# Kernel tuning notes

Hardware: AMD Instinct MI355X
Metric: run time of the kernel (lower is better)

## Reference

```python
import jax, jax.numpy as jnp
import numpy as np
import math

NB_STEPS = 50          # quadrature sub-intervals -> 51 Clenshaw-Curtis points
NUM_RNN_STEPS = 2


def _cc_weights(nb_steps):
    # Faithful port of UMNN's compute_cc_weights (Clenshaw-Curtis quadrature).
    lam = np.arange(0, nb_steps + 1).reshape(-1, 1).astype(np.float64)
    lam = np.cos((lam @ lam.T) * math.pi / nb_steps)
    lam[:, 0] = 0.5
    lam[:, -1] = 0.5 * lam[:, -1]
    lam = lam * 2.0 / nb_steps
    W = np.arange(0, nb_steps + 1).reshape(-1, 1).astype(np.float64)
    W[np.arange(1, nb_steps + 1, 2)] = 0
    W = 2.0 / (1.0 - W ** 2)
    W[0] = 1.0
    W[np.arange(1, nb_steps + 1, 2)] = 0
    cc = (lam.T @ W).astype(np.float32).reshape(-1)                      # [S]
    steps = np.cos(np.arange(0, nb_steps + 1) * math.pi / nb_steps).astype(np.float32)  # [S]
    return jnp.asarray(cc), jnp.asarray(steps)

CC_W, CC_STEPS = _cc_weights(NB_STEPS)  # S = NB_STEPS + 1 = 51


def _integrand(t, h, W1, b1, W2, b2, W3, b3, final_w):
    # IntegrandNN: MLP(cat(t,h)) -> ELU + 1 (>=0) -> fused power features -> ReLU(Linear)
    z = jnp.concatenate([t, h], axis=1)          # [N, in_d]
    z = jax.nn.relu(z @ W1.T + b1)               # [N, 128]
    z = jax.nn.relu(z @ W2.T + b2)               # [N, 128]
    z = jax.nn.elu(z @ W3.T + b3) + 1.0          # [N, 1], >= 0
    p = jnp.concatenate([z ** 1.5, z ** 2, z ** 2.5, z ** 3, z ** 3.5], axis=1)  # [N, 5]
    return jax.nn.relu((1.0 / (p + 1.0)) @ final_w.T)  # [N, 1]


def _inner_integral(x, h, params):
    # InnerUMNN: integral of IntegrandNN from x to xmax, xmax = max(x) + 10 (global scalar)
    N = x.shape[0]
    S = NB_STEPS + 1
    xmax = jnp.max(x) + 10.0
    T = x + (xmax - x) * (CC_STEPS[None, :] + 1.0) * 0.5   # [N, S]
    Tf = T.reshape(N * S, 1)
    hf = jnp.broadcast_to(h[:, None, :], (N, S, h.shape[1])).reshape(N * S, -1)
    g = _integrand(Tf, hf, *params).reshape(N, S)
    z = jnp.sum(g * CC_W[None, :], axis=1, keepdims=True)  # [N, 1]
    return z * (xmax - x) * 0.5


def _outer_integral(xT, h, params):
    # ParallelNeuralIntegral of InnerUMNN from x0 = 0 to xT; xT: [B, 1]
    B = xT.shape[0]
    S = NB_STEPS + 1
    X = xT * (CC_STEPS[None, :] + 1.0) * 0.5               # [B, S] (x0 = 0)
    Xf = X.reshape(B * S, 1)
    hf = jnp.broadcast_to(h[:, None, :], (B, S, h.shape[1])).reshape(B * S, -1)
    f = _inner_integral(Xf, hf, params).reshape(B, S)      # nested quadrature
    z = jnp.sum(f * CC_W[None, :], axis=1, keepdims=True)  # [B, 1]
    return z * xT * 0.5


def setup_inputs() -> dict:
    key = jax.random.key(0)
    ks = jax.random.split(key, 8)
    B, NF, IN_D, H = 256, 512, 64, 128
    x_ = jax.random.normal(ks[0], (B, NF), jnp.float32)
    h_ = jax.random.normal(ks[1], (B, IN_D - 1), jnp.float32)

    def lin(k, o, i):
        lim = 1.0 / np.sqrt(i)
        kw, kb = jax.random.split(k)
        return (jax.random.uniform(kw, (o, i), jnp.float32, -lim, lim),
                jax.random.uniform(kb, (o,), jnp.float32, -lim, lim))

    W1, b1 = lin(ks[2], H, IN_D)
    W2, b2 = lin(ks[3], H, H)
    W3, b3 = lin(ks[4], 1, H)
    lim5 = 1.0 / np.sqrt(5.0)
    final_w = jnp.abs(jax.random.uniform(ks[5], (1, 5), jnp.float32, -lim5, lim5))  # reset_params: abs
    log_weight = jnp.ones((1, NF), jnp.float32)            # reset_parameters: all ones
    sigmoid_param = jax.random.normal(ks[6], (1,), jnp.float32)
    return dict(x_=x_, h_=h_, W1=W1, b1=b1, W2=W2, b2=b2, W3=W3, b3=b3,
                final_w=final_w, log_weight=log_weight, sigmoid_param=sigmoid_param)


def reference(x_, h_, W1, b1, W2, b2, W3, b3, final_w, log_weight, sigmoid_param):
    params = (W1, b1, W2, b2, W3, b3, final_w)
    # compute_modular_function: F.linear then sum over dim 1 -> [B, 1]
    xm = jnp.sum(x_ @ log_weight.T, axis=1, keepdims=True)
    lam = jax.nn.sigmoid(sigmoid_param)                    # [1]
    out = jnp.zeros_like(xm)
    for _ in range(NUM_RNN_STEPS):
        xT = (1.0 - lam) * xm + lam * out
        out = _outer_integral(xT, h_, params)
    return out
```

## Files before the change

kernel.cpp:

```cpp
#include <hip/hip_runtime.h>
#include <math.h>

#define BB 256
#define NF 512
#define IND 64
#define HD 128
#define SS 51
#define NHM1 63

#define WS_LAM  0
#define WS_CCW  16
#define WS_U    80
#define WS_XM   144
#define WS_OUT1 656
#define WSH_C1  2048
#define WSH_W1  34816
#define WSH_W2F 40960

typedef _Float16 f16x2 __attribute__((ext_vector_type(2)));
typedef _Float16 f16x8 __attribute__((ext_vector_type(8)));
typedef float    f32x16 __attribute__((ext_vector_type(16)));

union f16x8_split { f16x8 v8; f16x2 v2[4]; };

__global__ void k_setup(const float* __restrict__ x_, const float* __restrict__ h_,
                        const float* __restrict__ W1, const float* __restrict__ b1,
                        const float* __restrict__ W2, const float* __restrict__ lw,
                        const float* __restrict__ sp, float* __restrict__ ws) {
    int b = blockIdx.x;
    int j = threadIdx.x;
    short* wsh = (short*)ws;

    float acc = b1[j];
    const float* w1row = W1 + j * IND;
    const float* hrow  = h_ + b * NHM1;
    #pragma unroll 7
    for (int k = 0; k < NHM1; ++k) acc = fmaf(w1row[1 + k], hrow[k], acc);
    {
        _Float16 hv = (_Float16)acc;
        short sv; __builtin_memcpy(&sv, &hv, 2);
        wsh[WSH_C1 + b * HD + j] = sv;
    }

    float s = 0.f;
    for (int k = j; k < NF; k += HD) s = fmaf(x_[b * NF + k], lw[k], s);
    __shared__ float red[HD];
    red[j] = s;
    __syncthreads();
    for (int off = 64; off > 0; off >>= 1) {
        if (j < off) red[j] += red[j + off];
        __syncthreads();
    }
    if (j == 0) ws[WS_XM + b] = red[0];

    if (b < 128) {
        int d = b * 128 + j;
        int i = d & 7, lane = (d >> 3) & 63, kn = d >> 9;
        int kk = kn >> 2, nt = kn & 3;
        int row = nt * 32 + (lane & 31);
        int k = kk * 16 + (lane >> 5) * 8 + i;
        _Float16 hv = (_Float16)W2[row * HD + k];
        short sv; __builtin_memcpy(&sv, &hv, 2);
        wsh[WSH_W2F + d] = sv;
    }

    if (b == 0) {
        if (j < SS) {
            float acc2 = 0.f;
            for (int jj = 0; jj <= 50; jj += 2) {
                float wj = (jj == 0) ? 1.f : 2.f / (1.f - (float)(jj * jj));
                float lamv;
                if (j == 0 || j == 50) {
                    lamv = 0.02f;
                } else {
                    int m = (jj * j) % 100;
                    lamv = cosf((float)m * (float)M_PI / 50.f) * 0.04f;
                }
                acc2 = fmaf(lamv, wj, acc2);
            }
            ws[WS_CCW + j] = acc2;
            float st = cosf((float)j * (float)M_PI / 50.f);
            ws[WS_U + j] = (st + 1.f) * 0.5f;
        }
        if (j == 127) ws[WS_LAM] = 1.f / (1.f + expf(-sp[0]));
    }
    if (b == 2) {
        _Float16 hv = (_Float16)W1[j * IND];
        short sv; __builtin_memcpy(&sv, &hv, 2);
        wsh[WSH_W1 + j] = sv;
    }
    if (b == 4) ws[WS_OUT1 + j] = 0.f;
    if (b == 5) ws[WS_OUT1 + 128 + j] = 0.f;
}

__launch_bounds__(256, 1)
__global__ void k_int(const float* __restrict__ b2, const float* __restrict__ W3,
                      const float* __restrict__ b3, const float* __restrict__ fw,
                      const float* __restrict__ ws, const float* __restrict__ outprev,
                      float* __restrict__ tgt, float* __restrict__ ztgt) {
    int b = blockIdx.x;
    int tid = threadIdx.x;
    int wv = tid >> 6, l = tid & 63;
    int e32 = l & 31, h2 = l >> 5;

    __shared__ float us[SS], ccs[SS], xw[4];

    if (ztgt && tid == 0) ztgt[b] = 0.f;
    if (tid < SS) { us[tid] = ws[WS_U + tid]; ccs[tid] = ws[WS_CCW + tid]; }

    float lam = ws[WS_LAM];
    float xmv = ws[WS_XM + tid];
    float opv = outprev ? outprev[tid] : 0.f;
    float xtv = (1.f - lam) * xmv + lam * opv;
    float mx = fmaxf(xtv, 0.f);
    #pragma unroll
    for (int off = 32; off >= 1; off >>= 1) mx = fmaxf(mx, __shfl_xor(mx, off, 64));
    if (l == 0) xw[wv] = mx;
    __syncthreads();
    float xmax = fmaxf(fmaxf(xw[0], xw[1]), fmaxf(xw[2], xw[3])) + 10.f;
    float xT = (1.f - lam) * ws[WS_XM + b] + lam * (outprev ? outprev[b] : 0.f);

    const short* wsh = (const short*)ws;

    f16x8 Af[8][4];
    #pragma unroll
    for (int kk = 0; kk < 8; ++kk)
        #pragma unroll
        for (int nt = 0; nt < 4; ++nt)
            Af[kk][nt] = *reinterpret_cast<const f16x8*>(
                wsh + WSH_W2F + ((kk * 4 + nt) * 64 + l) * 8);

    f16x2 c1p[8][4], w1p[8][4];
    #pragma unroll
    for (int kk = 0; kk < 8; ++kk) {
        f16x8_split c8, w8;
        c8.v8 = *reinterpret_cast<const f16x8*>(wsh + WSH_C1 + b * HD + kk * 16 + h2 * 8);
        w8.v8 = *reinterpret_cast<const f16x8*>(wsh + WSH_W1 + kk * 16 + h2 * 8);
        #pragma unroll
        for (int p = 0; p < 4; ++p) { c1p[kk][p] = c8.v2[p]; w1p[kk][p] = w8.v2[p]; }
    }

    float b2n[4][16], w3n[4][16];
    #pragma unroll
    for (int nt = 0; nt < 4; ++nt)
        #pragma unroll
        for (int r = 0; r < 16; ++r) {
            int j = nt * 32 + (r & 3) + 8 * (r >> 2) + 4 * h2;
            b2n[nt][r] = b2[j]; w3n[nt][r] = W3[j];
        }
    float b3v = b3[0];
    float fw0 = fw[0], fw1 = fw[1], fw2 = fw[2], fw3 = fw[3], fw4 = fw[4];

    float accO = 0.f;
    float zs_prev = 0.f, w_prev = 0.f;

    #pragma unroll 1
    for (int it = 0; it < 21; ++it) {
        int m = (wv * 21 + it) * 32 + e32;
        int valid = (m <= 2600);
        int mm = valid ? m : 2600;
        int s  = (mm * 41121) >> 21;
        int si = mm - s * 51;
        float x = xT * us[s];
        float range = xmax - x;
        float t = fmaf(range, us[si], x);
        float wgt = valid ? (ccs[si] * ccs[s] * range * xT * 0.25f) : 0.f;
        float wsel = h2 ? 0.f : wgt;
        _Float16 th = (_Float16)t;
        f16x2 tv = {th, th};

        f32x16 C0, C1, C2, C3;
        #pragma unroll
        for (int e = 0; e < 16; ++e) {
            C0[e] = b2n[0][e]; C1[e] = b2n[1][e];
            C2[e] = b2n[2][e]; C3[e] = b2n[3][e];
        }

        {
            float z = zs_prev > 0.f ? zs_prev + 1.f : __expf(zs_prev);
            float sq = sqrtf(z);
            float p15 = z * sq, p2 = z * z, p25 = p2 * sq, p3 = p2 * z, p35 = p3 * sq;
            float g = fw0 * __builtin_amdgcn_rcpf(p15 + 1.f)
                    + fw1 * __builtin_amdgcn_rcpf(p2  + 1.f)
                    + fw2 * __builtin_amdgcn_rcpf(p25 + 1.f)
                    + fw3 * __builtin_amdgcn_rcpf(p3  + 1.f)
                    + fw4 * __builtin_amdgcn_rcpf(p35 + 1.f);
            g = fmaxf(g, 0.f);
            accO = fmaf(g, w_prev, accO);
        }

        const f16x2 z2 = {(_Float16)0.f, (_Float16)0.f};
        #pragma unroll
        for (int kk = 0; kk < 8; ++kk) {
            f16x8_split Bu;
            #pragma unroll
            for (int p = 0; p < 4; ++p)
                Bu.v2[p] = __builtin_elementwise_max(
                    __builtin_elementwise_fma(w1p[kk][p], tv, c1p[kk][p]), z2);
            C0 = __builtin_amdgcn_mfma_f32_32x32x16_f16(Af[kk][0], Bu.v8, C0, 0, 0, 0);
            C1 = __builtin_amdgcn_mfma_f32_32x32x16_f16(Af[kk][1], Bu.v8, C1, 0, 0, 0);
            C2 = __builtin_amdgcn_mfma_f32_32x32x16_f16(Af[kk][2], Bu.v8, C2, 0, 0, 0);
            C3 = __builtin_amdgcn_mfma_f32_32x32x16_f16(Af[kk][3], Bu.v8, C3, 0, 0, 0);
        }

        float pa = 0.f, pb = 0.f, pc = 0.f, pd = 0.f;
        #pragma unroll
        for (int r = 0; r < 16; ++r) {
            pa = fmaf(fmaxf(C0[r], 0.f), w3n[0][r], pa);
            pb = fmaf(fmaxf(C1[r], 0.f), w3n[1][r], pb);
            pc = fmaf(fmaxf(C2[r], 0.f), w3n[2][r], pc);
            pd = fmaf(fmaxf(C3[r], 0.f), w3n[3][r], pd);
        }
        float z1 = (pa + pb) + (pc + pd);
        z1 += __shfl_xor(z1, 32, 64);
        zs_prev = z1 + b3v;
        w_prev = wsel;
    }

    {
        float z = zs_prev > 0.f ? zs_prev + 1.f : __expf(zs_prev);
        float sq = sqrtf(z);
        float p15 = z * sq, p2 = z * z, p25 = p2 * sq, p3 = p2 * z, p35 = p3 * sq;
        float g = fw0 * __builtin_amdgcn_rcpf(p15 + 1.f)
                + fw1 * __builtin_amdgcn_rcpf(p2  + 1.f)
                + fw2 * __builtin_amdgcn_rcpf(p25 + 1.f)
                + fw3 * __builtin_amdgcn_rcpf(p3  + 1.f)
                + fw4 * __builtin_amdgcn_rcpf(p35 + 1.f);
        g = fmaxf(g, 0.f);
        accO = fmaf(g, w_prev, accO);
    }

    #pragma unroll
    for (int off = 32; off >= 1; off >>= 1) accO += __shfl_xor(accO, off, 64);
    if (l == 0) atomicAdd(&tgt[b], accO);
}

extern "C" void kernel_launch(void* const* d_in, const int* in_sizes, int n_in,
                              void* d_out, int out_size, void* d_ws, size_t ws_size,
                              hipStream_t stream) {
    (void)in_sizes; (void)n_in; (void)out_size; (void)ws_size;
    const float* x_ = (const float*)d_in[0];
    const float* h_ = (const float*)d_in[1];
    const float* W1 = (const float*)d_in[2];
    const float* b1 = (const float*)d_in[3];
    const float* W2 = (const float*)d_in[4];
    const float* b2 = (const float*)d_in[5];
    const float* W3 = (const float*)d_in[6];
    const float* b3 = (const float*)d_in[7];
    const float* fw = (const float*)d_in[8];
    const float* lw = (const float*)d_in[9];
    const float* sp = (const float*)d_in[10];
    float* wsf  = (float*)d_ws;
    float* out1 = wsf + WS_OUT1;
    float* out  = (float*)d_out;

    k_setup<<<BB, HD, 0, stream>>>(x_, h_, W1, b1, W2, lw, sp, wsf);
    k_int<<<BB, 256, 0, stream>>>(b2, W3, b3, fw, wsf, nullptr, out1, out);
    k_int<<<BB, 256, 0, stream>>>(b2, W3, b3, fw, wsf, out1, out, nullptr);
}
```

Before: 73.16 us.

## Split integrand work across wave pairs and double the grid

Each k_int block now covers half of a batch row's quadrature points, and the grid doubles to 512 blocks. Within a block, pairs of waves split the four 32-column output tiles of the W2 GEMM and exchange partial sums through shared memory with a per-iteration barrier. The bias and W3 epilogue moves to packed fp16 with dot2, and the layer-1 weights come from LDS instead of registers. The aim is to cut register pressure so two blocks fit per CU and to spread work over more CUs, at the cost of a __syncthreads per iteration and lower epilogue precision.

New measurement: 81.46 us. 1.11x slower.

```diff
diff --git a/kernel.cpp b/kernel.cpp
--- a/kernel.cpp
+++ b/kernel.cpp
@@ -18,10 +18,25 @@
 #define WSH_W2F 40960
 
 typedef _Float16 f16x2 __attribute__((ext_vector_type(2)));
+typedef __fp16   fp16x2 __attribute__((ext_vector_type(2)));
 typedef _Float16 f16x8 __attribute__((ext_vector_type(8)));
 typedef float    f32x16 __attribute__((ext_vector_type(16)));
 
 union f16x8_split { f16x8 v8; f16x2 v2[4]; };
+union pk_cast { fp16x2 p; f16x2 f; };
+
+static __device__ inline f16x2 cvt_pk(float a, float b) {
+    pk_cast u; u.p = __builtin_amdgcn_cvt_pkrtz(a, b);
+    return u.f;
+}
+
+static __device__ inline float dot2f(f16x2 a, f16x2 b, float c) {
+#if __has_builtin(__builtin_amdgcn_fdot2)
+    return __builtin_amdgcn_fdot2(a, b, c, false);
+#else
+    return c + (float)a[0] * (float)b[0] + (float)a[1] * (float)b[1];
+#endif
+}
 
 __global__ void k_setup(const float* __restrict__ x_, const float* __restrict__ h_,
                         const float* __restrict__ W1, const float* __restrict__ b1,
@@ -93,20 +108,27 @@
     if (b == 5) ws[WS_OUT1 + 128 + j] = 0.f;
 }
 
-__launch_bounds__(256, 1)
+__launch_bounds__(256, 2)
 __global__ void k_int(const float* __restrict__ b2, const float* __restrict__ W3,
                       const float* __restrict__ b3, const float* __restrict__ fw,
                       const float* __restrict__ ws, const float* __restrict__ outprev,
                       float* __restrict__ tgt, float* __restrict__ ztgt) {
-    int b = blockIdx.x;
+    int b = blockIdx.x >> 1, hf = blockIdx.x & 1;
     int tid = threadIdx.x;
     int wv = tid >> 6, l = tid & 63;
     int e32 = l & 31, h2 = l >> 5;
+    int pi = wv & 1, ps = wv >> 1;
 
     __shared__ float us[SS], ccs[SS], xw[4];
-
-    if (ztgt && tid == 0) ztgt[b] = 0.f;
+    __shared__ short c1h[HD], w1h[HD];
+    __shared__ float part[2][2][2][32];
+
+    if (ztgt && hf == 0 && tid == 0) ztgt[b] = 0.f;
     if (tid < SS) { us[tid] = ws[WS_U + tid]; ccs[tid] = ws[WS_CCW + tid]; }
+    {
+        const short* wsh0 = (const short*)ws;
+        if (tid < HD) { c1h[tid] = wsh0[WSH_C1 + b * HD + tid]; w1h[tid] = wsh0[WSH_W1 + tid]; }
+    }
 
     float lam = ws[WS_LAM];
     float xmv = ws[WS_XM + tid];
@@ -122,41 +144,39 @@
 
     const short* wsh = (const short*)ws;
 
-    f16x8 Af[8][4];
+    f16x8 Af[8][2];
     #pragma unroll
     for (int kk = 0; kk < 8; ++kk)
         #pragma unroll
-        for (int nt = 0; nt < 4; ++nt)
-            Af[kk][nt] = *reinterpret_cast<const f16x8*>(
-                wsh + WSH_W2F + ((kk * 4 + nt) * 64 + l) * 8);
-
-    f16x2 c1p[8][4], w1p[8][4];
-    #pragma unroll
-    for (int kk = 0; kk < 8; ++kk) {
-        f16x8_split c8, w8;
-        c8.v8 = *reinterpret_cast<const f16x8*>(wsh + WSH_C1 + b * HD + kk * 16 + h2 * 8);
-        w8.v8 = *reinterpret_cast<const f16x8*>(wsh + WSH_W1 + kk * 16 + h2 * 8);
-        #pragma unroll
-        for (int p = 0; p < 4; ++p) { c1p[kk][p] = c8.v2[p]; w1p[kk][p] = w8.v2[p]; }
-    }
-
-    float b2n[4][16], w3n[4][16];
-    #pragma unroll
-    for (int nt = 0; nt < 4; ++nt)
-        #pragma unroll
-        for (int r = 0; r < 16; ++r) {
-            int j = nt * 32 + (r & 3) + 8 * (r >> 2) + 4 * h2;
-            b2n[nt][r] = b2[j]; w3n[nt][r] = W3[j];
-        }
+        for (int u = 0; u < 2; ++u) {
+            int ntg = 2 * pi + u;
+            Af[kk][u] = *reinterpret_cast<const f16x8*>(
+                wsh + WSH_W2F + ((kk * 4 + ntg) * 64 + l) * 8);
+        }
+
+    f16x2 b2pk[2][8], w3pk[2][8];
+    #pragma unroll
+    for (int u = 0; u < 2; ++u) {
+        int jb = (2 * pi + u) * 32;
+        #pragma unroll
+        for (int q = 0; q < 8; ++q) {
+            int r0 = ((2 * q) & 3) + 8 * ((2 * q) >> 2) + 4 * h2;
+            b2pk[u][q] = cvt_pk(b2[jb + r0], b2[jb + r0 + 1]);
+            w3pk[u][q] = cvt_pk(W3[jb + r0], W3[jb + r0 + 1]);
+        }
+    }
     float b3v = b3[0];
     float fw0 = fw[0], fw1 = fw[1], fw2 = fw[2], fw3 = fw[3], fw4 = fw[4];
 
     float accO = 0.f;
     float zs_prev = 0.f, w_prev = 0.f;
+    int buf = 0;
+    const f16x2 z2 = {(_Float16)0.f, (_Float16)0.f};
 
     #pragma unroll 1
     for (int it = 0; it < 21; ++it) {
-        int m = (wv * 21 + it) * 32 + e32;
+        int tl = hf * 42 + ps * 21 + it;
+        int m = tl * 32 + e32;
         int valid = (m <= 2600);
         int mm = valid ? m : 2600;
         int s  = (mm * 41121) >> 21;
@@ -165,16 +185,13 @@
         float range = xmax - x;
         float t = fmaf(range, us[si], x);
         float wgt = valid ? (ccs[si] * ccs[s] * range * xT * 0.25f) : 0.f;
-        float wsel = h2 ? 0.f : wgt;
+        float wsel = (h2 == 0 && (e32 >> 4) == pi) ? wgt : 0.f;
         _Float16 th = (_Float16)t;
         f16x2 tv = {th, th};
 
-        f32x16 C0, C1, C2, C3;
-        #pragma unroll
-        for (int e = 0; e < 16; ++e) {
-            C0[e] = b2n[0][e]; C1[e] = b2n[1][e];
-            C2[e] = b2n[2][e]; C3[e] = b2n[3][e];
-        }
+        f32x16 C0, C1;
+        #pragma unroll
+        for (int e = 0; e < 16; ++e) { C0[e] = 0.f; C1[e] = 0.f; }
 
         {
             float z = zs_prev > 0.f ? zs_prev + 1.f : __expf(zs_prev);
@@ -189,32 +206,37 @@
             accO = fmaf(g, w_prev, accO);
         }
 
-        const f16x2 z2 = {(_Float16)0.f, (_Float16)0.f};
         #pragma unroll
         for (int kk = 0; kk < 8; ++kk) {
-            f16x8_split Bu;
+            f16x8_split c8, w8, Bu;
+            c8.v8 = *reinterpret_cast<const f16x8*>(&c1h[kk * 16 + h2 * 8]);
+            w8.v8 = *reinterpret_cast<const f16x8*>(&w1h[kk * 16 + h2 * 8]);
             #pragma unroll
             for (int p = 0; p < 4; ++p)
                 Bu.v2[p] = __builtin_elementwise_max(
-                    __builtin_elementwise_fma(w1p[kk][p], tv, c1p[kk][p]), z2);
+                    __builtin_elementwise_fma(w8.v2[p], tv, c8.v2[p]), z2);
             C0 = __builtin_amdgcn_mfma_f32_32x32x16_f16(Af[kk][0], Bu.v8, C0, 0, 0, 0);
             C1 = __builtin_amdgcn_mfma_f32_32x32x16_f16(Af[kk][1], Bu.v8, C1, 0, 0, 0);
-            C2 = __builtin_amdgcn_mfma_f32_32x32x16_f16(Af[kk][2], Bu.v8, C2, 0, 0, 0);
-            C3 = __builtin_amdgcn_mfma_f32_32x32x16_f16(Af[kk][3], Bu.v8, C3, 0, 0, 0);
-        }
-
-        float pa = 0.f, pb = 0.f, pc = 0.f, pd = 0.f;
-        #pragma unroll
-        for (int r = 0; r < 16; ++r) {
-            pa = fmaf(fmaxf(C0[r], 0.f), w3n[0][r], pa);
-            pb = fmaf(fmaxf(C1[r], 0.f), w3n[1][r], pb);
-            pc = fmaf(fmaxf(C2[r], 0.f), w3n[2][r], pc);
-            pd = fmaf(fmaxf(C3[r], 0.f), w3n[3][r], pd);
-        }
-        float z1 = (pa + pb) + (pc + pd);
-        z1 += __shfl_xor(z1, 32, 64);
-        zs_prev = z1 + b3v;
+        }
+
+        float za = 0.f, zb = 0.f;
+        #pragma unroll
+        for (int q = 0; q < 8; ++q) {
+            f16x2 a0 = cvt_pk(C0[2 * q], C0[2 * q + 1]);
+            a0 = __builtin_elementwise_max(a0 + b2pk[0][q], z2);
+            za = dot2f(a0, w3pk[0][q], za);
+            f16x2 a1 = cvt_pk(C1[2 * q], C1[2 * q + 1]);
+            a1 = __builtin_elementwise_max(a1 + b2pk[1][q], z2);
+            zb = dot2f(a1, w3pk[1][q], zb);
+        }
+        float zhalf = za + zb;
+        zhalf += __shfl_xor(zhalf, 32, 64);
+        if (h2 == 0) part[ps][pi][buf][e32] = zhalf;
+        __syncthreads();
+        float zoth = part[ps][pi ^ 1][buf][e32];
+        zs_prev = zhalf + zoth + b3v;
         w_prev = wsel;
+        buf ^= 1;
     }
 
     {
@@ -255,6 +277,6 @@
     float* out  = (float*)d_out;
 
     k_setup<<<BB, HD, 0, stream>>>(x_, h_, W1, b1, W2, lw, sp, wsf);
-    k_int<<<BB, 256, 0, stream>>>(b2, W3, b3, fw, wsf, nullptr, out1, out);
-    k_int<<<BB, 256, 0, stream>>>(b2, W3, b3, fw, wsf, out1, out, nullptr);
-}
+    k_int<<<BB * 2, 256, 0, stream>>>(b2, W3, b3, fw, wsf, nullptr, out1, out);
+    k_int<<<BB * 2, 256, 0, stream>>>(b2, W3, b3, fw, wsf, out1, out, nullptr);
+}
```
